# Kernel tuning notes

Measured on AMD Instinct MI355X. Metric: run time of the kernel, lower is better.

Reference implementation:

```python
import jax, jax.numpy as jnp
import numpy as np

N = 100000         # nodes
E = 800000         # directed edges (before self loops)
F_IN = 64          # num_node_features
HID = 128          # hidden_channels
HEADS = 4
HD = HID // HEADS  # head_dim = 32
NEG_SLOPE = 0.2    # GATv2Conv default negative_slope


def _layernorm(x, g, b, eps=1e-5):
    m = jnp.mean(x, axis=-1, keepdims=True)
    v = jnp.var(x, axis=-1, keepdims=True)
    return (x - m) * jax.lax.rsqrt(v + eps) * g + b


def _gatv2_conv(x, src, dst, w_l, w_r, att, heads, hd):
    # GATv2Conv (share_weights=False, bias=False, concat=True), inference mode.
    n = x.shape[0]
    x_l = (x @ w_l).reshape(n, heads, hd)   # source-side transform
    x_r = (x @ w_r).reshape(n, heads, hd)   # target-side transform
    x_j = x_l[src]                          # [Et, H, C] gather (messages)
    e = jax.nn.leaky_relu(x_j + x_r[dst], NEG_SLOPE)
    logits = jnp.einsum('ehc,hc->eh', e, att)            # [Et, H]
    m = jax.ops.segment_max(logits, dst, num_segments=n)  # stable segment softmax
    p = jnp.exp(logits - m[dst])
    s = jax.ops.segment_sum(p, dst, num_segments=n)
    alpha = p / s[dst]
    out = jax.ops.segment_sum(x_j * alpha[..., None], dst, num_segments=n)
    return out.reshape(n, heads * hd)


def _forward(edge_index, x, ln_in_g, ln_in_b, w_l1, w_r1, att1, ln1_g, ln1_b,
             w_l2, w_r2, att2, ln2_g, ln2_b, w_l3, w_r3, att3, ln3_g, ln3_b,
             rtt_w1, rtt_b1, rtt_w2, rtt_b2, ret_w1, ret_b1, ret_w2, ret_b2):
    n = x.shape[0]
    loops = jnp.arange(n, dtype=edge_index.dtype)
    src = jnp.concatenate([edge_index[0], loops])  # add_self_loops=True
    dst = jnp.concatenate([edge_index[1], loops])
    h = _layernorm(x, ln_in_g, ln_in_b)
    # layer 0: F_IN -> HID (4 heads), no residual (dims differ)
    h = _gatv2_conv(h, src, dst, w_l1, w_r1, att1, HEADS, HD)
    h = jax.nn.relu(_layernorm(h, ln1_g, ln1_b))
    # layer 1: HID -> HID (4 heads), residual * 0.1
    res = h
    h = _gatv2_conv(h, src, dst, w_l2, w_r2, att2, HEADS, HD)
    h = jax.nn.relu(_layernorm(h, ln2_g, ln2_b) + 0.1 * res)
    # layer 2: HID -> HID (1 head), residual * 0.1, no relu (last layer)
    res = h
    h = _gatv2_conv(h, src, dst, w_l3, w_r3, att3, 1, HID)
    h = _layernorm(h, ln3_g, ln3_b) + 0.1 * res
    # prediction heads (dropout inactive at inference)
    rtt = jax.nn.relu(h @ rtt_w1 + rtt_b1) @ rtt_w2 + rtt_b2
    ret = jax.nn.relu(h @ ret_w1 + ret_b1) @ ret_w2 + ret_b2
    return jnp.concatenate([rtt, ret], axis=1)  # [N, 2]


def setup_inputs() -> dict:
    key = jax.random.key(0)
    ks = jax.random.split(key, 32)

    def xavier(k, shape, gain=0.3):
        lim = gain * np.sqrt(6.0 / (shape[0] + shape[1]))
        return jax.random.uniform(k, shape, jnp.float32, -lim, lim)

    inp = {
        'x': jax.random.normal(ks[0], (N, F_IN), jnp.float32),
        'edge_index': jax.random.randint(ks[1], (2, E), 0, N, jnp.int32),
        'ln_in_g': jnp.ones((F_IN,), jnp.float32),
        'ln_in_b': jnp.zeros((F_IN,), jnp.float32),
        'w_l1': xavier(ks[2], (F_IN, HID)),
        'w_r1': xavier(ks[3], (F_IN, HID)),
        'att1': jax.random.normal(ks[4], (HEADS, HD), jnp.float32) * 0.1,
        'ln1_g': jnp.ones((HID,), jnp.float32),
        'ln1_b': jnp.zeros((HID,), jnp.float32),
        'w_l2': xavier(ks[5], (HID, HID)),
        'w_r2': xavier(ks[6], (HID, HID)),
        'att2': jax.random.normal(ks[7], (HEADS, HD), jnp.float32) * 0.1,
        'ln2_g': jnp.ones((HID,), jnp.float32),
        'ln2_b': jnp.zeros((HID,), jnp.float32),
        'w_l3': xavier(ks[8], (HID, HID)),
        'w_r3': xavier(ks[9], (HID, HID)),
        'att3': jax.random.normal(ks[10], (1, HID), jnp.float32) * 0.1,
        'ln3_g': jnp.ones((HID,), jnp.float32),
        'ln3_b': jnp.zeros((HID,), jnp.float32),
        'rtt_w1': xavier(ks[11], (HID, HID // 2)),
        'rtt_b1': jnp.zeros((HID // 2,), jnp.float32),
        'rtt_w2': xavier(ks[12], (HID // 2, 1)),
        'rtt_b2': jnp.zeros((1,), jnp.float32),
        'ret_w1': xavier(ks[13], (HID, HID // 2)),
        'ret_b1': jnp.zeros((HID // 2,), jnp.float32),
        'ret_w2': xavier(ks[14], (HID // 2, 1)),
        'ret_b2': jnp.zeros((1,), jnp.float32),
    }
    return inp


def reference(x, edge_index, ln_in_g, ln_in_b, w_l1, w_r1, att1, ln1_g, ln1_b,
              w_l2, w_r2, att2, ln2_g, ln2_b, w_l3, w_r3, att3, ln3_g, ln3_b,
              rtt_w1, rtt_b1, rtt_w2, rtt_b2, ret_w1, ret_b1, ret_w2, ret_b2):
    return _forward(edge_index, x, ln_in_g, ln_in_b, w_l1, w_r1, att1, ln1_g,
                    ln1_b, w_l2, w_r2, att2, ln2_g, ln2_b, w_l3, w_r3, att3,
                    ln3_g, ln3_b, rtt_w1, rtt_b1, rtt_w2, rtt_b2, ret_w1,
                    ret_b1, ret_w2, ret_b2)
```

## Files before the change

kernel.cpp:

```cpp
#include <hip/hip_runtime.h>
#include <hip/hip_bf16.h>
#include <cstdint>
#include <cstddef>

#define NEG_SLOPE 0.2f

typedef float f4v __attribute__((ext_vector_type(4)));
typedef float f8v __attribute__((ext_vector_type(8)));
typedef _Float16 h8v __attribute__((ext_vector_type(8)));
typedef float f32x4 __attribute__((ext_vector_type(4)));

__device__ __forceinline__ void cvt2h(float v, _Float16& h, _Float16& l) {
  h = (_Float16)v;
  l = (_Float16)(v - (float)h);
}


__global__ __launch_bounds__(256) void degree_count_kernel(
    const int* __restrict__ ei, int E, int* __restrict__ deg) {
  int e = blockIdx.x * 256 + threadIdx.x;
  if (e < E) atomicAdd(&deg[ei[E + e]], 1);
}

__global__ __launch_bounds__(1024) void scan1_kernel(
    const int* __restrict__ deg, int n, int* __restrict__ incl,
    int* __restrict__ blocksums) {
  __shared__ int sm[1024];
  int t = threadIdx.x;
  int i = blockIdx.x * 1024 + t;
  sm[t] = (i < n) ? (deg[i] + 1) : 0;
  __syncthreads();
  #pragma unroll
  for (int o = 1; o < 1024; o <<= 1) {
    int a = (t >= o) ? sm[t - o] : 0;
    __syncthreads();
    sm[t] += a;
    __syncthreads();
  }
  if (i < n) incl[i] = sm[t];
  if (t == 1023) blocksums[blockIdx.x] = sm[t];
}

__global__ __launch_bounds__(1024) void scan23_kernel(
    const int* __restrict__ incl, const int* __restrict__ deg,
    const int* __restrict__ bs, int nb, int n, int* __restrict__ rowcur) {
  int i = blockIdx.x * 1024 + threadIdx.x;
  if (i >= n) return;
  int off = 0;
  for (int j = 0; j < (int)blockIdx.x; j++) off += bs[j];
  rowcur[i] = incl[i] - (deg[i] + 1) + off;
}

__global__ __launch_bounds__(256) void scatter_kernel(
    const int* __restrict__ ei, int E, int ET, int* __restrict__ rowcur,
    int* __restrict__ csr_src) {
  int e = blockIdx.x * 256 + threadIdx.x;
  if (e >= ET) return;
  int s, d;
  if (e < E) { s = ei[e]; d = ei[E + e]; }
  else       { s = e - E; d = s; }
  int pos = atomicAdd(&rowcur[d], 1);
  csr_src[pos] = s;
}

struct PrepArgs {
  const float* w[8];
  short* o[8];
  int fout[8];
  int cum[9];
};

__global__ __launch_bounds__(256) void prep_w_kernel(PrepArgs pa) {
  int i = blockIdx.x * 256 + threadIdx.x;
  if (i >= pa.cum[8]) return;
  int s = 0;
  while (i >= pa.cum[s + 1]) s++;
  int li = i - pa.cum[s];
  int FOUT = pa.fout[s];
  int NT = FOUT >> 4;
  int sz = pa.cum[s + 1] - pa.cum[s];
  int c = li / (NT * 512);
  int r1 = li % (NT * 512);
  int t = r1 >> 9;
  int e = r1 & 511;
  int lane = e >> 3, j = e & 7;
  int k = c * 32 + (lane >> 4) * 8 + j;
  int n = t * 16 + (lane & 15);
  float v = pa.w[s][k * FOUT + n];
  _Float16 h, l;
  cvt2h(v, h, l);
  pa.o[s][li] = __builtin_bit_cast(short, h);
  pa.o[s][li + sz] = __builtin_bit_cast(short, l);
}

#define MFMA3H(ah, al, bh, bl, acc)                                          \
  acc = __builtin_amdgcn_mfma_f32_16x16x32_f16(ah, bh, acc, 0, 0, 0);       \
  acc = __builtin_amdgcn_mfma_f32_16x16x32_f16(ah, bl, acc, 0, 0, 0);       \
  acc = __builtin_amdgcn_mfma_f32_16x16x32_f16(al, bh, acc, 0, 0, 0);

#define MFMA2H(ah, bh, bl, acc)                                              \
  acc = __builtin_amdgcn_mfma_f32_16x16x32_f16(ah, bh, acc, 0, 0, 0);       \
  acc = __builtin_amdgcn_mfma_f32_16x16x32_f16(ah, bl, acc, 0, 0, 0);

__global__ __launch_bounds__(256, 4) void mfma_gemm_ln_kernel(
    const float* __restrict__ X, const float* __restrict__ lng,
    const float* __restrict__ lnb, const short* __restrict__ WfL,
    const short* __restrict__ WfR, _Float16* __restrict__ YL,
    _Float16* __restrict__ YR, int nrows) {
  constexpr int NT = 8, TOT = 2 * NT * 512;
  const short* Wf = blockIdx.y ? WfR : WfL;
  _Float16* Y = blockIdx.y ? YR : YL;
  const int wave = threadIdx.x >> 6, lane = threadIdx.x & 63;
  const int quad = lane >> 4, ln16 = lane & 15;
  const int rb = blockIdx.x * 64 + wave * 16;
  int r0 = rb + ln16;
  int rA0 = r0 < nrows ? r0 : nrows - 1;
  const float* xp0 = X + (size_t)rA0 * 64 + quad * 8;

  float av[16];
  *(float4*)&av[0]  = *(const float4*)(xp0);
  *(float4*)&av[4]  = *(const float4*)(xp0 + 4);
  *(float4*)&av[8]  = *(const float4*)(xp0 + 32);
  *(float4*)&av[12] = *(const float4*)(xp0 + 36);

  float s0 = 0.f, q0 = 0.f;
  #pragma unroll
  for (int j = 0; j < 16; j++) {
    s0 += av[j]; q0 += av[j] * av[j];
  }
  s0 += __shfl_xor(s0, 16); s0 += __shfl_xor(s0, 32);
  q0 += __shfl_xor(q0, 16); q0 += __shfl_xor(q0, 32);
  float mean0 = s0 * (1.f / 64.f);
  float rstd0 = rsqrtf(q0 * (1.f / 64.f) - mean0 * mean0 + 1e-5f);

  f32x4 acc[NT];
  #pragma unroll
  for (int t = 0; t < NT; t++) acc[t] = (f32x4){0.f, 0.f, 0.f, 0.f};

  #pragma unroll
  for (int c = 0; c < 2; c++) {
    float4 gv0 = *(const float4*)&lng[quad * 8 + c * 32];
    float4 gv1 = *(const float4*)&lng[quad * 8 + c * 32 + 4];
    float4 bv0 = *(const float4*)&lnb[quad * 8 + c * 32];
    float4 bv1 = *(const float4*)&lnb[quad * 8 + c * 32 + 4];
    float gg[8] = {gv0.x, gv0.y, gv0.z, gv0.w, gv1.x, gv1.y, gv1.z, gv1.w};
    float bb[8] = {bv0.x, bv0.y, bv0.z, bv0.w, bv1.x, bv1.y, bv1.z, bv1.w};
    h8v ah, al;
    #pragma unroll
    for (int j = 0; j < 8; j++) {
      float v0 = (av[c * 8 + j] - mean0) * rstd0 * gg[j] + bb[j];
      _Float16 h, l;
      cvt2h(v0, h, l); ah[j] = h; al[j] = l;
    }
    const short* wp = Wf + c * NT * 512 + lane * 8;
    #pragma unroll
    for (int t = 0; t < NT; t++) {
      h8v bh = *(const h8v*)(wp + t * 512);
      h8v bl = *(const h8v*)(wp + t * 512 + TOT);
      MFMA3H(ah, al, bh, bl, acc[t]);
    }
  }

  const int rbase = rb + quad * 4;
  #pragma unroll
  for (int t = 0; t < NT; t++)
    #pragma unroll
    for (int r = 0; r < 4; r++) {
      int ra = rbase + r;
      if (ra < nrows) Y[(size_t)ra * 128 + t * 16 + ln16] = (_Float16)acc[t][r];
    }
}

__global__ __launch_bounds__(256, 4) void mfma_gemm_lr_kernel(
    const _Float16* __restrict__ X, const short* __restrict__ WfL,
    const short* __restrict__ WfR, _Float16* __restrict__ YL,
    _Float16* __restrict__ YR, int nrows) {
  constexpr int NC = 4, NT = 8, TOT = NC * NT * 512;
  const short* Wf = blockIdx.y ? WfR : WfL;
  _Float16* Y = blockIdx.y ? YR : YL;
  const int wave = threadIdx.x >> 6, lane = threadIdx.x & 63;
  const int quad = lane >> 4, ln16 = lane & 15;
  const int rb = blockIdx.x * 64 + wave * 16;
  int r0 = rb + ln16;
  int rA0 = r0 < nrows ? r0 : nrows - 1;
  const _Float16* xp0 = X + (size_t)rA0 * 128 + quad * 8;

  f32x4 acc[NT];
  #pragma unroll
  for (int t = 0; t < NT; t++) acc[t] = (f32x4){0.f, 0.f, 0.f, 0.f};

  #pragma unroll
  for (int c = 0; c < NC; c++) {
    h8v ah = *(const h8v*)(xp0 + c * 32);
    const short* wp = Wf + c * NT * 512 + lane * 8;
    #pragma unroll
    for (int t = 0; t < NT; t++) {
      h8v bh = *(const h8v*)(wp + t * 512);
      h8v bl = *(const h8v*)(wp + t * 512 + TOT);
      MFMA2H(ah, bh, bl, acc[t]);
    }
  }

  const int rbase = rb + quad * 4;
  #pragma unroll
  for (int t = 0; t < NT; t++)
    #pragma unroll
    for (int r = 0; r < 4; r++) {
      int ra = rbase + r;
      if (ra < nrows) Y[(size_t)ra * 128 + t * 16 + ln16] = (_Float16)acc[t][r];
    }
}

__global__ __launch_bounds__(256, 2) void mfma_head_lr_kernel(
    const _Float16* __restrict__ X, const short* __restrict__ Wf1,
    const float* __restrict__ b1a, const float* __restrict__ w2a,
    const float* __restrict__ b2a, const short* __restrict__ Wf2,
    const float* __restrict__ b1b, const float* __restrict__ w2b,
    const float* __restrict__ b2b, float* __restrict__ out, int nrows) {
  constexpr int NC = 4, NT = 4, TOT = NC * NT * 512;
  const int wave = threadIdx.x >> 6, lane = threadIdx.x & 63;
  const int quad = lane >> 4, ln16 = lane & 15;
  int rowA = blockIdx.x * 64 + wave * 16 + ln16;
  int rA = rowA < nrows ? rowA : nrows - 1;
  const _Float16* xp = X + (size_t)rA * 128 + quad * 8;

  f32x4 accL[NT], accR[NT];
  #pragma unroll
  for (int t = 0; t < NT; t++) {
    accL[t] = (f32x4){0.f, 0.f, 0.f, 0.f};
    accR[t] = (f32x4){0.f, 0.f, 0.f, 0.f};
  }

  #pragma unroll
  for (int c = 0; c < NC; c++) {
    h8v ah = *(const h8v*)(xp + c * 32);
    const short* wpL = Wf1 + c * NT * 512 + lane * 8;
    const short* wpR = Wf2 + c * NT * 512 + lane * 8;
    #pragma unroll
    for (int t = 0; t < NT; t++) {
      h8v bh = *(const h8v*)(wpL + t * 512);
      h8v bl = *(const h8v*)(wpL + t * 512 + TOT);
      MFMA2H(ah, bh, bl, accL[t]);
      h8v ch = *(const h8v*)(wpR + t * 512);
      h8v cl = *(const h8v*)(wpR + t * 512 + TOT);
      MFMA2H(ah, ch, cl, accR[t]);
    }
  }

  float prA[4] = {0.f, 0.f, 0.f, 0.f};
  float prB[4] = {0.f, 0.f, 0.f, 0.f};
  #pragma unroll
  for (int t = 0; t < NT; t++) {
    float bvA = b1a[t * 16 + ln16], wvA = w2a[t * 16 + ln16];
    float bvB = b1b[t * 16 + ln16], wvB = w2b[t * 16 + ln16];
    #pragma unroll
    for (int r = 0; r < 4; r++) {
      prA[r] += fmaxf(accL[t][r] + bvA, 0.f) * wvA;
      prB[r] += fmaxf(accR[t][r] + bvB, 0.f) * wvB;
    }
  }
  #pragma unroll
  for (int o = 1; o < 16; o <<= 1)
    #pragma unroll
    for (int r = 0; r < 4; r++) {
      prA[r] += __shfl_xor(prA[r], o);
      prB[r] += __shfl_xor(prB[r], o);
    }
  if (ln16 == 0) {
    const float bb2a = b2a[0], bb2b = b2b[0];
    const int rbase = blockIdx.x * 64 + wave * 16 + quad * 4;
    #pragma unroll
    for (int r = 0; r < 4; r++) {
      int rr = rbase + r;
      if (rr < nrows) {
        out[(size_t)rr * 2 + 0] = prA[r] + bb2a;
        out[(size_t)rr * 2 + 1] = prB[r] + bb2b;
      }
    }
  }
}

template <int H>
__global__ __launch_bounds__(64) void gat_fused_kernel(
    const _Float16* __restrict__ xl, const _Float16* __restrict__ xr,
    const int* __restrict__ csr_src, const int* __restrict__ row_end,
    const int* __restrict__ deg, const float* __restrict__ att,
    const _Float16* __restrict__ res, const float* __restrict__ g,
    const float* __restrict__ b, _Float16* __restrict__ y, int n,
    float resScale, int doRelu) {
  int l = threadIdx.x & 63;
  int rh = l >> 5;
  int st = (l >> 4) & 1;
  int ln = l & 15;
  int row = blockIdx.x * 2 + rh;
  int rowC = row < n ? row : n - 1;
  int cb = ln * 32;
  int cbh = ln * 16;
  int end = row_end[rowC];
  int dg = deg[rowC] + 1;
  int start = end - dg;
  int cnt = (dg - st + 1) >> 1;

  h8v xrh = *(const h8v*)((const char*)xr + (size_t)rowC * 256 + cbh);
  f8v xrf = __builtin_convertvector(xrh, f8v);
  f4v av0 = *(const f4v*)((const char*)att + cb);
  f4v av1 = *(const f4v*)((const char*)att + cb + 16);

  float s = 0.f;
  float ac[8] = {0.f, 0.f, 0.f, 0.f, 0.f, 0.f, 0.f, 0.f};

  int idx = start + st;
  h8v pa = (h8v)0, pb = (h8v)0;
  if (cnt > 0)
    pa = *(const h8v*)((const char*)xl + (size_t)csr_src[idx] * 256 + cbh);
  if (cnt > 1)
    pb = *(const h8v*)((const char*)xl + (size_t)csr_src[idx + 2] * 256 + cbh);
  for (int i = 0; i < cnt; i++) {
    f8v xv = __builtin_convertvector(pa, f8v);
    pa = pb;
    if (i + 2 < cnt)
      pb = *(const h8v*)((const char*)xl + (size_t)csr_src[idx + 4] * 256 + cbh);
    idx += 2;
    float p0;
    {
      float t0 = xv[0] + xrf[0], t1 = xv[1] + xrf[1];
      float t2 = xv[2] + xrf[2], t3 = xv[3] + xrf[3];
      float t4 = xv[4] + xrf[4], t5 = xv[5] + xrf[5];
      float t6 = xv[6] + xrf[6], t7 = xv[7] + xrf[7];
      float v0 = fmaxf(t0, NEG_SLOPE * t0), v1 = fmaxf(t1, NEG_SLOPE * t1);
      float v2 = fmaxf(t2, NEG_SLOPE * t2), v3 = fmaxf(t3, NEG_SLOPE * t3);
      float v4 = fmaxf(t4, NEG_SLOPE * t4), v5 = fmaxf(t5, NEG_SLOPE * t5);
      float v6 = fmaxf(t6, NEG_SLOPE * t6), v7 = fmaxf(t7, NEG_SLOPE * t7);
      p0 = v0 * av0.x + v1 * av0.y + v2 * av0.z + v3 * av0.w +
           v4 * av1.x + v5 * av1.y + v6 * av1.z + v7 * av1.w;
    }
    if constexpr (H == 1) {
      #pragma unroll
      for (int o = 1; o < 16; o <<= 1) p0 += __shfl_xor(p0, o);
    } else {
      p0 += __shfl_xor(p0, 1);
      p0 += __shfl_xor(p0, 2);
    }
    float e = __expf(p0);
    s += e;
    ac[0] += e * xv[0]; ac[1] += e * xv[1];
    ac[2] += e * xv[2]; ac[3] += e * xv[3];
    ac[4] += e * xv[4]; ac[5] += e * xv[5];
    ac[6] += e * xv[6]; ac[7] += e * xv[7];
  }
  s += __shfl_xor(s, 16);
  #pragma unroll
  for (int j = 0; j < 8; j++) ac[j] += __shfl_xor(ac[j], 16);

  float inv = 1.f / s;
  float ov[8];
  #pragma unroll
  for (int j = 0; j < 8; j++) ov[j] = ac[j] * inv;

  float sum = 0.f, sq = 0.f;
  #pragma unroll
  for (int j = 0; j < 8; j++) { sum += ov[j]; sq += ov[j] * ov[j]; }
  #pragma unroll
  for (int o = 1; o < 16; o <<= 1) {
    sum += __shfl_xor(sum, o);
    sq += __shfl_xor(sq, o);
  }
  float mean = sum * (1.f / 128.f);
  float var = sq * (1.f / 128.f) - mean * mean;
  float rstd = rsqrtf(var + 1e-5f);

  f4v gv0 = *(const f4v*)((const char*)g + cb);
  f4v gv1 = *(const f4v*)((const char*)g + cb + 16);
  f4v bv0 = *(const f4v*)((const char*)b + cb);
  f4v bv1 = *(const f4v*)((const char*)b + cb + 16);
  float gg[8] = {gv0.x, gv0.y, gv0.z, gv0.w, gv1.x, gv1.y, gv1.z, gv1.w};
  float bb[8] = {bv0.x, bv0.y, bv0.z, bv0.w, bv1.x, bv1.y, bv1.z, bv1.w};
  float rv[8];
  #pragma unroll
  for (int j = 0; j < 8; j++) rv[j] = (ov[j] - mean) * rstd * gg[j] + bb[j];
  if (res) {
    h8v rr = *(const h8v*)((const char*)res + (size_t)rowC * 256 + cbh);
    f8v rf = __builtin_convertvector(rr, f8v);
    #pragma unroll
    for (int j = 0; j < 8; j++) rv[j] += resScale * rf[j];
  }
  if (doRelu) {
    #pragma unroll
    for (int j = 0; j < 8; j++) rv[j] = fmaxf(rv[j], 0.f);
  }
  if (st == 0 && row < n) {
    f8v of;
    #pragma unroll
    for (int j = 0; j < 8; j++) of[j] = rv[j];
    h8v oh = __builtin_convertvector(of, h8v);
    *(h8v*)((char*)y + (size_t)row * 256 + cbh) = oh;
  }
}

extern "C" void kernel_launch(void* const* d_in, const int* in_sizes, int n_in,
                              void* d_out, int out_size, void* d_ws,
                              size_t ws_size, hipStream_t stream) {
  const float* x       = (const float*)d_in[0];
  const int*   ei      = (const int*)d_in[1];
  const float* ln_in_g = (const float*)d_in[2];
  const float* ln_in_b = (const float*)d_in[3];
  const float* w_l1    = (const float*)d_in[4];
  const float* w_r1    = (const float*)d_in[5];
  const float* att1    = (const float*)d_in[6];
  const float* ln1_g   = (const float*)d_in[7];
  const float* ln1_b   = (const float*)d_in[8];
  const float* w_l2    = (const float*)d_in[9];
  const float* w_r2    = (const float*)d_in[10];
  const float* att2    = (const float*)d_in[11];
  const float* ln2_g   = (const float*)d_in[12];
  const float* ln2_b   = (const float*)d_in[13];
  const float* w_l3    = (const float*)d_in[14];
  const float* w_r3    = (const float*)d_in[15];
  const float* att3    = (const float*)d_in[16];
  const float* ln3_g   = (const float*)d_in[17];
  const float* ln3_b   = (const float*)d_in[18];
  const float* rtt_w1  = (const float*)d_in[19];
  const float* rtt_b1  = (const float*)d_in[20];
  const float* rtt_w2  = (const float*)d_in[21];
  const float* rtt_b2  = (const float*)d_in[22];
  const float* ret_w1  = (const float*)d_in[23];
  const float* ret_b1  = (const float*)d_in[24];
  const float* ret_w2  = (const float*)d_in[25];
  const float* ret_b2  = (const float*)d_in[26];

  const int N = in_sizes[0] / 64;
  const int E = in_sizes[1] / 2;
  const int ET = E + N;
  const size_t NF = (size_t)N * 128;

  _Float16* A = (_Float16*)d_ws;
  _Float16* B = A + NF;
  _Float16* C = B + NF;
  int* deg     = (int*)(C + NF);
  int* rowcur  = deg + N;
  int* incl    = rowcur + N;
  int* bsums   = incl + N;
  int* csr_src = bsums + 1024;
  short* wf = (short*)(((uintptr_t)(csr_src + ET) + 63) & ~(uintptr_t)63);

  float* out = (float*)d_out;

  const int segsz[8] = {64 * 128, 64 * 128, 128 * 128, 128 * 128,
                        128 * 128, 128 * 128, 128 * 64, 128 * 64};
  PrepArgs pa;
  pa.w[0] = w_l1; pa.w[1] = w_r1; pa.w[2] = w_l2; pa.w[3] = w_r2;
  pa.w[4] = w_l3; pa.w[5] = w_r3; pa.w[6] = rtt_w1; pa.w[7] = ret_w1;
  pa.fout[0] = 128; pa.fout[1] = 128; pa.fout[2] = 128; pa.fout[3] = 128;
  pa.fout[4] = 128; pa.fout[5] = 128; pa.fout[6] = 64; pa.fout[7] = 64;
  int acc = 0;
  short* op = wf;
  for (int s = 0; s < 8; s++) {
    pa.cum[s] = acc;
    pa.o[s] = op;
    op += 2 * segsz[s];
    acc += segsz[s];
  }
  pa.cum[8] = acc;

  const int mmBlocks   = (N + 63) / 64;
  const int gatBlocks  = (N + 1) / 2;
  const int NB = (N + 1023) / 1024;
  dim3 lrGrid(mmBlocks, 2);

  prep_w_kernel<<<(acc + 255) / 256, 256, 0, stream>>>(pa);

  hipMemsetAsync(deg, 0, (size_t)N * sizeof(int), stream);
  degree_count_kernel<<<(E + 255) / 256, 256, 0, stream>>>(ei, E, deg);
  scan1_kernel<<<NB, 1024, 0, stream>>>(deg, N, incl, bsums);
  scan23_kernel<<<NB, 1024, 0, stream>>>(incl, deg, bsums, NB, N, rowcur);
  scatter_kernel<<<(ET + 255) / 256, 256, 0, stream>>>(ei, E, ET, rowcur, csr_src);

  mfma_gemm_ln_kernel<<<lrGrid, 256, 0, stream>>>(
      x, ln_in_g, ln_in_b, pa.o[0], pa.o[1], B, C, N);
  gat_fused_kernel<4><<<gatBlocks, 64, 0, stream>>>(
      B, C, csr_src, rowcur, deg, att1, nullptr, ln1_g, ln1_b, A, N, 0.f, 1);

  mfma_gemm_lr_kernel<<<lrGrid, 256, 0, stream>>>(A, pa.o[2], pa.o[3], B, C, N);
  gat_fused_kernel<4><<<gatBlocks, 64, 0, stream>>>(
      B, C, csr_src, rowcur, deg, att2, A, ln2_g, ln2_b, A, N, 0.1f, 1);

  mfma_gemm_lr_kernel<<<lrGrid, 256, 0, stream>>>(A, pa.o[4], pa.o[5], B, C, N);
  gat_fused_kernel<1><<<gatBlocks, 64, 0, stream>>>(
      B, C, csr_src, rowcur, deg, att3, A, ln3_g, ln3_b, A, N, 0.1f, 0);

  mfma_head_lr_kernel<<<mmBlocks, 256, 0, stream>>>(
      A, pa.o[6], rtt_b1, rtt_w2, rtt_b2, pa.o[7], ret_b1, ret_w2, ret_b2,
      out, N);
}
```

Baseline: 503.5 us.

## Merge CSR build kernels: fuse weight prep with degree, scatter with first LN-GEMM

Fuses the weight-prep kernel with the degree-count kernel in one launch and records each edge's atomic rank there. The CSR scatter then needs no second atomic: it writes to rowstart+rank, and it runs as extra blocks inside the first LayerNorm+GEMM kernel, so two launches are removed. The GAT kernels now read row starts directly instead of deriving them from row ends. The cost is an extra rank array of E ints to write and read. Mixing different block types in one grid may also unbalance scheduling, and the first GEMM now waits for the scan to finish.

```diff
diff --git a/kernel.cpp b/kernel.cpp
--- a/kernel.cpp
+++ b/kernel.cpp
@@ -15,11 +15,41 @@
   l = (_Float16)(v - (float)h);
 }
 
-
-__global__ __launch_bounds__(256) void degree_count_kernel(
-    const int* __restrict__ ei, int E, int* __restrict__ deg) {
-  int e = blockIdx.x * 256 + threadIdx.x;
-  if (e < E) atomicAdd(&deg[ei[E + e]], 1);
+struct PrepArgs {
+  const float* w[8];
+  short* o[8];
+  int fout[8];
+  int cum[9];
+};
+
+__global__ __launch_bounds__(256) void prep_degree_kernel(
+    PrepArgs pa, int prepBlocks, const int* __restrict__ ei, int E,
+    int* __restrict__ deg, int* __restrict__ rank) {
+  if ((int)blockIdx.x < prepBlocks) {
+    int i = blockIdx.x * 256 + threadIdx.x;
+    if (i >= pa.cum[8]) return;
+    int s = 0;
+    while (i >= pa.cum[s + 1]) s++;
+    int li = i - pa.cum[s];
+    int FOUT = pa.fout[s];
+    int NT = FOUT >> 4;
+    int sz = pa.cum[s + 1] - pa.cum[s];
+    int c = li / (NT * 512);
+    int r1 = li % (NT * 512);
+    int t = r1 >> 9;
+    int e = r1 & 511;
+    int lane = e >> 3, j = e & 7;
+    int k = c * 32 + (lane >> 4) * 8 + j;
+    int n = t * 16 + (lane & 15);
+    float v = pa.w[s][k * FOUT + n];
+    _Float16 h, l;
+    cvt2h(v, h, l);
+    pa.o[s][li] = __builtin_bit_cast(short, h);
+    pa.o[s][li + sz] = __builtin_bit_cast(short, l);
+  } else {
+    int e = ((int)blockIdx.x - prepBlocks) * 256 + threadIdx.x;
+    if (e < E) rank[e] = atomicAdd(&deg[ei[E + e]], 1);
+  }
 }
 
 __global__ __launch_bounds__(1024) void scan1_kernel(
@@ -43,54 +73,12 @@
 
 __global__ __launch_bounds__(1024) void scan23_kernel(
     const int* __restrict__ incl, const int* __restrict__ deg,
-    const int* __restrict__ bs, int nb, int n, int* __restrict__ rowcur) {
+    const int* __restrict__ bs, int nb, int n, int* __restrict__ rowstart) {
   int i = blockIdx.x * 1024 + threadIdx.x;
   if (i >= n) return;
   int off = 0;
   for (int j = 0; j < (int)blockIdx.x; j++) off += bs[j];
-  rowcur[i] = incl[i] - (deg[i] + 1) + off;
-}
-
-__global__ __launch_bounds__(256) void scatter_kernel(
-    const int* __restrict__ ei, int E, int ET, int* __restrict__ rowcur,
-    int* __restrict__ csr_src) {
-  int e = blockIdx.x * 256 + threadIdx.x;
-  if (e >= ET) return;
-  int s, d;
-  if (e < E) { s = ei[e]; d = ei[E + e]; }
-  else       { s = e - E; d = s; }
-  int pos = atomicAdd(&rowcur[d], 1);
-  csr_src[pos] = s;
-}
-
-struct PrepArgs {
-  const float* w[8];
-  short* o[8];
-  int fout[8];
-  int cum[9];
-};
-
-__global__ __launch_bounds__(256) void prep_w_kernel(PrepArgs pa) {
-  int i = blockIdx.x * 256 + threadIdx.x;
-  if (i >= pa.cum[8]) return;
-  int s = 0;
-  while (i >= pa.cum[s + 1]) s++;
-  int li = i - pa.cum[s];
-  int FOUT = pa.fout[s];
-  int NT = FOUT >> 4;
-  int sz = pa.cum[s + 1] - pa.cum[s];
-  int c = li / (NT * 512);
-  int r1 = li % (NT * 512);
-  int t = r1 >> 9;
-  int e = r1 & 511;
-  int lane = e >> 3, j = e & 7;
-  int k = c * 32 + (lane >> 4) * 8 + j;
-  int n = t * 16 + (lane & 15);
-  float v = pa.w[s][k * FOUT + n];
-  _Float16 h, l;
-  cvt2h(v, h, l);
-  pa.o[s][li] = __builtin_bit_cast(short, h);
-  pa.o[s][li + sz] = __builtin_bit_cast(short, l);
+  rowstart[i] = incl[i] - (deg[i] + 1) + off;
 }
 
 #define MFMA3H(ah, al, bh, bl, acc)                                          \
@@ -102,17 +90,33 @@
   acc = __builtin_amdgcn_mfma_f32_16x16x32_f16(ah, bh, acc, 0, 0, 0);       \
   acc = __builtin_amdgcn_mfma_f32_16x16x32_f16(ah, bl, acc, 0, 0, 0);
 
-__global__ __launch_bounds__(256, 4) void mfma_gemm_ln_kernel(
+__global__ __launch_bounds__(256, 4) void ln_scatter_kernel(
     const float* __restrict__ X, const float* __restrict__ lng,
     const float* __restrict__ lnb, const short* __restrict__ WfL,
     const short* __restrict__ WfR, _Float16* __restrict__ YL,
-    _Float16* __restrict__ YR, int nrows) {
+    _Float16* __restrict__ YR, int nrows, int lnB,
+    const int* __restrict__ ei, int E, int ET,
+    const int* __restrict__ rowstart, const int* __restrict__ rank,
+    const int* __restrict__ deg, int* __restrict__ csr_src) {
+  int b = blockIdx.x;
+  if (b >= 2 * lnB) {
+    int e = (b - 2 * lnB) * 256 + threadIdx.x;
+    if (e < ET) {
+      int s, d, r;
+      if (e < E) { s = ei[e]; d = ei[E + e]; r = rank[e]; }
+      else       { s = e - E; d = s; r = deg[d]; }
+      csr_src[rowstart[d] + r] = s;
+    }
+    return;
+  }
   constexpr int NT = 8, TOT = 2 * NT * 512;
-  const short* Wf = blockIdx.y ? WfR : WfL;
-  _Float16* Y = blockIdx.y ? YR : YL;
+  const int side = (b >= lnB);
+  const int bx = b - side * lnB;
+  const short* Wf = side ? WfR : WfL;
+  _Float16* Y = side ? YR : YL;
   const int wave = threadIdx.x >> 6, lane = threadIdx.x & 63;
   const int quad = lane >> 4, ln16 = lane & 15;
-  const int rb = blockIdx.x * 64 + wave * 16;
+  const int rb = bx * 64 + wave * 16;
   int r0 = rb + ln16;
   int rA0 = r0 < nrows ? r0 : nrows - 1;
   const float* xp0 = X + (size_t)rA0 * 64 + quad * 8;
@@ -283,7 +287,7 @@
 template <int H>
 __global__ __launch_bounds__(64) void gat_fused_kernel(
     const _Float16* __restrict__ xl, const _Float16* __restrict__ xr,
-    const int* __restrict__ csr_src, const int* __restrict__ row_end,
+    const int* __restrict__ csr_src, const int* __restrict__ row_start,
     const int* __restrict__ deg, const float* __restrict__ att,
     const _Float16* __restrict__ res, const float* __restrict__ g,
     const float* __restrict__ b, _Float16* __restrict__ y, int n,
@@ -296,9 +300,8 @@
   int rowC = row < n ? row : n - 1;
   int cb = ln * 32;
   int cbh = ln * 16;
-  int end = row_end[rowC];
+  int start = row_start[rowC];
   int dg = deg[rowC] + 1;
-  int start = end - dg;
   int cnt = (dg - st + 1) >> 1;
 
   h8v xrh = *(const h8v*)((const char*)xr + (size_t)rowC * 256 + cbh);
@@ -436,12 +439,13 @@
   _Float16* A = (_Float16*)d_ws;
   _Float16* B = A + NF;
   _Float16* C = B + NF;
-  int* deg     = (int*)(C + NF);
-  int* rowcur  = deg + N;
-  int* incl    = rowcur + N;
-  int* bsums   = incl + N;
-  int* csr_src = bsums + 1024;
-  short* wf = (short*)(((uintptr_t)(csr_src + ET) + 63) & ~(uintptr_t)63);
+  int* deg      = (int*)(C + NF);
+  int* rowstart = deg + N;
+  int* incl     = rowstart + N;
+  int* bsums    = incl + N;
+  int* csr_src  = bsums + 1024;
+  int* rank     = csr_src + ET;
+  short* wf = (short*)(((uintptr_t)(rank + E) + 63) & ~(uintptr_t)63);
 
   float* out = (float*)d_out;
 
@@ -465,28 +469,30 @@
   const int mmBlocks   = (N + 63) / 64;
   const int gatBlocks  = (N + 1) / 2;
   const int NB = (N + 1023) / 1024;
+  const int prepBlocks = (acc + 255) / 256;
+  const int degBlocks  = (E + 255) / 256;
+  const int scatBlocks = (ET + 255) / 256;
   dim3 lrGrid(mmBlocks, 2);
 
-  prep_w_kernel<<<(acc + 255) / 256, 256, 0, stream>>>(pa);
-
   hipMemsetAsync(deg, 0, (size_t)N * sizeof(int), stream);
-  degree_count_kernel<<<(E + 255) / 256, 256, 0, stream>>>(ei, E, deg);
+  prep_degree_kernel<<<prepBlocks + degBlocks, 256, 0, stream>>>(
+      pa, prepBlocks, ei, E, deg, rank);
   scan1_kernel<<<NB, 1024, 0, stream>>>(deg, N, incl, bsums);
-  scan23_kernel<<<NB, 1024, 0, stream>>>(incl, deg, bsums, NB, N, rowcur);
-  scatter_kernel<<<(ET + 255) / 256, 256, 0, stream>>>(ei, E, ET, rowcur, csr_src);
-
-  mfma_gemm_ln_kernel<<<lrGrid, 256, 0, stream>>>(
-      x, ln_in_g, ln_in_b, pa.o[0], pa.o[1], B, C, N);
+  scan23_kernel<<<NB, 1024, 0, stream>>>(incl, deg, bsums, NB, N, rowstart);
+
+  ln_scatter_kernel<<<2 * mmBlocks + scatBlocks, 256, 0, stream>>>(
+      x, ln_in_g, ln_in_b, pa.o[0], pa.o[1], B, C, N, mmBlocks,
+      ei, E, ET, rowstart, rank, deg, csr_src);
   gat_fused_kernel<4><<<gatBlocks, 64, 0, stream>>>(
-      B, C, csr_src, rowcur, deg, att1, nullptr, ln1_g, ln1_b, A, N, 0.f, 1);
+      B, C, csr_src, rowstart, deg, att1, nullptr, ln1_g, ln1_b, A, N, 0.f, 1);
 
   mfma_gemm_lr_kernel<<<lrGrid, 256, 0, stream>>>(A, pa.o[2], pa.o[3], B, C, N);
   gat_fused_kernel<4><<<gatBlocks, 64, 0, stream>>>(
-      B, C, csr_src, rowcur, deg, att2, A, ln2_g, ln2_b, A, N, 0.1f, 1);
+      B, C, csr_src, rowstart, deg, att2, A, ln2_g, ln2_b, A, N, 0.1f, 1);
 
   mfma_gemm_lr_kernel<<<lrGrid, 256, 0, stream>>>(A, pa.o[4], pa.o[5], B, C, N);
   gat_fused_kernel<1><<<gatBlocks, 64, 0, stream>>>(
-      B, C, csr_src, rowcur, deg, att3, A, ln3_g, ln3_b, A, N, 0.1f, 0);
+      B, C, csr_src, rowstart, deg, att3, A, ln3_g, ln3_b, A, N, 0.1f, 0);
 
   mfma_head_lr_kernel<<<mmBlocks, 256, 0, stream>>>(
       A, pa.o[6], rtt_b1, rtt_w2, rtt_b2, pa.o[7], ret_b1, ret_w2, ret_b2,
```

Result: faster. 451.7 us (-10.3%).
